# Kernel optimization log

Hardware: AMD Instinct MI355X
Metric: run time of the kernel (lower is better)

The kernel has to match this reference:

```python
import jax, jax.numpy as jnp
import numpy as np

DIM = 1024
NUM_HEADS = 16
WINDOW_SIZE = 512
HEAD_DIM = DIM // NUM_HEADS
SCALE = HEAD_DIM ** (-0.5)


def setup_inputs() -> dict:
    key = jax.random.key(0)
    kq, kk, kv = jax.random.split(key, 3)
    shape = (2, NUM_HEADS, 2048, HEAD_DIM)
    q = jax.random.normal(kq, shape, dtype=jnp.float32)
    k = jax.random.normal(kk, shape, dtype=jnp.float32)
    v = jax.random.normal(kv, shape, dtype=jnp.float32)
    return {"q": q, "k": k, "v": v}


def reference(q, k, v):
    B, H, N, D = q.shape
    pos = jnp.arange(N)
    # causal + sliding window: col <= row and col >= row - w + 1
    window_mask = (pos[None, :] <= pos[:, None]) & (pos[None, :] >= pos[:, None] - WINDOW_SIZE + 1)  # (N, N)
    attn = jnp.einsum("bhnd,bhmd->bhnm", q, k) * SCALE  # (B, H, N, N)
    attn = jnp.where(window_mask[None, None], attn, -jnp.inf)
    attn = jax.nn.softmax(attn, axis=-1)
    attn = jnp.nan_to_num(attn, nan=0.0)
    return jnp.einsum("bhnm,bhmd->bhnd", attn, v)
```

## Files before the change

### kernel.cpp

```cpp
#include <hip/hip_runtime.h>
#include <math.h>


#define SEQ 2048
#define HD  64
#define LDR 72

typedef short short8 __attribute__((ext_vector_type(8)));
typedef float f32x4  __attribute__((ext_vector_type(4)));

static __device__ inline unsigned short f2bf(float f){
  union{float f; unsigned u;} un; un.f=f;
  return (unsigned short)((un.u + 0x7FFFu + ((un.u>>16)&1u))>>16);
}
static __device__ inline int swz(int row){ return (row&3)|(((row>>3)&1)<<2); }

static __device__ __forceinline__ void gll16(const unsigned short* g, unsigned short* l){
  __builtin_amdgcn_global_load_lds(
    (const __attribute__((address_space(1))) unsigned int*)(const void*)g,
    (__attribute__((address_space(3))) unsigned int*)(void*)l, 16, 0, 0);
}

__global__ __launch_bounds__(256) void swa_prep(
    const float* __restrict__ k, const float* __restrict__ v,
    unsigned short* __restrict__ Kb, unsigned short* __restrict__ Vtb)
{
  const int tid=threadIdx.x, bid=blockIdx.x;
  const float C=0.18033688011112042f;

  if(bid<1024){
    const long tbase=(long)bid*4096;
    #pragma unroll
    for(int i=0;i<2;++i){
      int id=i*256+tid, r=id>>3, lc=id&7;
      float4 f0=*(const float4*)(k+tbase+r*64+lc*8);
      float4 f1=*(const float4*)(k+tbase+r*64+lc*8+4);
      unsigned short hh[8];
      hh[0]=f2bf(f0.x*C); hh[1]=f2bf(f0.y*C); hh[2]=f2bf(f0.z*C); hh[3]=f2bf(f0.w*C);
      hh[4]=f2bf(f1.x*C); hh[5]=f2bf(f1.y*C); hh[6]=f2bf(f1.z*C); hh[7]=f2bf(f1.w*C);
      *(uint4*)(Kb+tbase+r*64+(long)((lc^swz(r))*8))=*(uint4*)hh;
    }
  } else {
    __shared__ unsigned short Vs[64*68];
    const long tbase=(long)(bid-1024)*4096;
    #pragma unroll
    for(int i=0;i<2;++i){
      int id=i*256+tid, r=id>>3, c=id&7;
      int phys=(c^(r>>3))&7;
      float4 f0=*(const float4*)(v+tbase+r*64+c*8);
      float4 f1=*(const float4*)(v+tbase+r*64+c*8+4);
      ushort4 a,b;
      a.x=f2bf(f0.x); a.y=f2bf(f0.y); a.z=f2bf(f0.z); a.w=f2bf(f0.w);
      b.x=f2bf(f1.x); b.y=f2bf(f1.y); b.z=f2bf(f1.z); b.w=f2bf(f1.w);
      *(ushort4*)&Vs[r*68+phys*8]  =a;
      *(ushort4*)&Vs[r*68+phys*8+4]=b;
    }
    __syncthreads();
    #pragma unroll
    for(int i=0;i<2;++i){
      int id=i*256+tid, d=id>>3, lc=id&7;
      unsigned short t8[8];
      #pragma unroll
      for(int e=0;e<8;++e){
        int key=lc*8+e;
        int phys=((d>>3)^lc)&7;
        t8[e]=Vs[key*68 + phys*8 + (d&7)];
      }
      *(uint4*)(Vtb+tbase+d*64+(long)((lc^swz(d))*8))=*(uint4*)t8;
    }
  }
}

__global__ __launch_bounds__(512) void swa_main(
    const float* __restrict__ q,
    const unsigned short* __restrict__ Kb,
    const unsigned short* __restrict__ Vtb,
    float* __restrict__ out)
{
  __shared__ unsigned short Ks[2][8192];
  __shared__ unsigned short Vsh[2][8192];

  const int tid=threadIdx.x, bid=blockIdx.x;
  const int mt=bid&15, bh=bid>>4, m0=mt*128;
  const long base=(long)bh*SEQ*HD;
  const int wv=tid>>6, lane=tid&63, quad=lane>>4, l16=lane&15;
  const int qrow=m0+wv*16+l16;
  const int h=wv>>2;

  short8 qa[2];
  {
    const float* qp=q+base+(long)qrow*HD+quad*8;
    #pragma unroll
    for(int kk=0;kk<2;++kk){
      float4 f0=*(const float4*)(qp+kk*32);
      float4 f1=*(const float4*)(qp+kk*32+4);
      short8 a;
      a[0]=(short)f2bf(f0.x); a[1]=(short)f2bf(f0.y);
      a[2]=(short)f2bf(f0.z); a[3]=(short)f2bf(f0.w);
      a[4]=(short)f2bf(f1.x); a[5]=(short)f2bf(f1.y);
      a[6]=(short)f2bf(f1.z); a[7]=(short)f2bf(f1.w);
      qa[kk]=a;
    }
  }

  const int rbase=8*(l16>>2)+(l16&3);
  const int swk=(l16&3)|(((l16>>2)&1)<<2);
  const int swv=(l16&3)|(((l16>>3)&1)<<2);
  int kaoff[2][4], vboff[2][4];
  #pragma unroll
  for(int kk=0;kk<2;++kk){
    #pragma unroll
    for(int nt=0;nt<4;++nt)
      kaoff[kk][nt]=(rbase+(nt&1)*4+(nt>>1)*32)*64+(((quad+4*kk)^swk)*8);
    #pragma unroll
    for(int dt=0;dt<4;++dt)
      vboff[kk][dt]=(dt*16+l16)*64+(((quad+4*kk)^swv)*8);
  }

  const unsigned short* Kt=Kb +(long)bh*32*4096;
  const unsigned short* Vt=Vtb+(long)bh*32*4096;
  const int seg=tid*8;

  f32x4 oacc[4];
  #pragma unroll
  for(int dt=0;dt<4;++dt) oacc[dt]=(f32x4){0.f,0.f,0.f,0.f};
  float lrun=0.f;

  const int Tb  =2*mt+1;
  const int Tlo =(2*mt>8)?(2*mt-8):0;
  const int npairs=(Tb-Tlo+1)>>1;
  const int myTb=2*mt+h;
  const int myTlo=(myTb>=8)?(myTb-8):0;
  const bool clip=(myTb>=8);

  {
    const long o=(long)Tlo*4096;
    gll16(Kt+o+seg,      &Ks[0][seg]);
    gll16(Kt+o+4096+seg, &Ks[0][4096+seg]);
    gll16(Vt+o+seg,      &Vsh[0][seg]);
    gll16(Vt+o+4096+seg, &Vsh[0][4096+seg]);
  }
  __syncthreads();

  for(int p=0;p<npairs;++p){
    const int buf=p&1;
    if(p+1<npairs){
      const long o=(long)(Tlo+2*(p+1))*4096;
      gll16(Kt+o+seg,      &Ks[buf^1][seg]);
      gll16(Kt+o+4096+seg, &Ks[buf^1][4096+seg]);
      gll16(Vt+o+seg,      &Vsh[buf^1][seg]);
      gll16(Vt+o+4096+seg, &Vsh[buf^1][4096+seg]);
    }
    #pragma unroll
    for(int sub=0;sub<2;++sub){
      const int t=Tlo+2*p+sub;
      if(t>=myTlo && t<=myTb){
        const int tb_off=sub*4096;
        f32x4 sacc[4];
        #pragma unroll
        for(int nt=0;nt<4;++nt) sacc[nt]=(f32x4){0.f,0.f,0.f,0.f};
        #pragma unroll
        for(int kk=0;kk<2;++kk){
          #pragma unroll
          for(int nt=0;nt<4;++nt){
            short8 ka=*(const short8*)&Ks[buf][tb_off+kaoff[kk][nt]];
            sacc[nt]=__builtin_amdgcn_mfma_f32_16x16x32_bf16(ka,qa[kk],sacc[nt],0,0,0);
          }
        }
        short8 vb[4][2];
        #pragma unroll
        for(int dt=0;dt<4;++dt)
          #pragma unroll
          for(int kk=0;kk<2;++kk)
            vb[dt][kk]=*(const short8*)&Vsh[buf][tb_off+vboff[kk][dt]];

        unsigned short pb[16];
        const bool msk=(t==myTb)||(clip&&t==myTlo);
        if(msk){
          #pragma unroll
          for(int nt=0;nt<4;++nt){
            #pragma unroll
            for(int r=0;r<4;++r){
              float e=__builtin_amdgcn_exp2f(sacc[nt][r]);
              int key=t*64+8*quad+r+(nt&1)*4+(nt>>1)*32;
              bool valid=(key<=qrow)&&(key+511>=qrow);
              e=valid?e:0.f;
              lrun+=e;
              pb[nt*4+r]=f2bf(e);
            }
          }
        } else {
          #pragma unroll
          for(int nt=0;nt<4;++nt){
            #pragma unroll
            for(int r=0;r<4;++r){
              float e=__builtin_amdgcn_exp2f(sacc[nt][r]);
              lrun+=e;
              pb[nt*4+r]=f2bf(e);
            }
          }
        }
        short8 pa0,pa1;
        #pragma unroll
        for(int j=0;j<8;++j){ pa0[j]=(short)pb[j]; pa1[j]=(short)pb[8+j]; }
        #pragma unroll
        for(int dt=0;dt<4;++dt){
          oacc[dt]=__builtin_amdgcn_mfma_f32_16x16x32_bf16(pa0,vb[dt][0],oacc[dt],0,0,0);
          oacc[dt]=__builtin_amdgcn_mfma_f32_16x16x32_bf16(pa1,vb[dt][1],oacc[dt],0,0,0);
        }
      }
    }
    __syncthreads();
  }

  lrun+=__shfl_xor(lrun,16);
  lrun+=__shfl_xor(lrun,32);
  float linv=1.0f/lrun;
  #pragma unroll
  for(int r=0;r<4;++r){
    float lr=__shfl(linv,quad*4+r);
    const int orow=m0+wv*16+quad*4+r;
    #pragma unroll
    for(int dt=0;dt<4;++dt)
      out[base+(long)orow*HD+dt*16+l16]=oacc[dt][r]*lr;
  }
}

__global__ __launch_bounds__(256) void swa_fwd(
    const float* __restrict__ q, const float* __restrict__ k,
    const float* __restrict__ v, float* __restrict__ out)
{
  __shared__ short Qs[64*LDR];
  __shared__ short Ps[64*LDR];
  __shared__ short Ksh[2][64*LDR];
  __shared__ short Vtr[2][HD*LDR];

  const int tid=threadIdx.x, bid=blockIdx.x;
  const int mtile=bid&31, bh=bid>>5, m0=mtile*64;
  const long base=(long)bh*SEQ*HD;
  const int wv=tid>>6, lane=tid&63, quad=lane>>4, l16=lane&15;
  const int dcol=lane;

  {
    const float4* qg=(const float4*)(q+base+(long)m0*HD);
    #pragma unroll
    for(int i=0;i<4;++i){
      int idx=i*256+tid, r=idx>>4, c4=idx&15;
      float4 f=qg[idx];
      ushort4 hh; hh.x=f2bf(f.x); hh.y=f2bf(f.y); hh.z=f2bf(f.z); hh.w=f2bf(f.w);
      *(ushort4*)&Qs[r*LDR+c4*4]=hh;
    }
  }
  const int tb=mtile, tlo=(tb>8)?(tb-8):0;
  float4 kreg[4]; float vcol[4][4];
  {
    const float4* kg=(const float4*)(k+base+(long)(tlo*64)*HD);
    const float*  vg=v+base+(long)(tlo*64)*HD;
    #pragma unroll
    for(int i=0;i<4;++i) kreg[i]=kg[i*256+tid];
    #pragma unroll
    for(int g=0;g<4;++g){ int r0=wv*4+g*16;
      #pragma unroll
      for(int j=0;j<4;++j) vcol[g][j]=vg[(r0+j)*HD+dcol]; }
  }
  __syncthreads();
  short8 qa[2];
  #pragma unroll
  for(int kk=0;kk<2;++kk)
    qa[kk]=*(const short8*)&Qs[(wv*16+l16)*LDR+kk*32+quad*8];
  {
    #pragma unroll
    for(int i=0;i<4;++i){
      int idx=i*256+tid, r=idx>>4, c4=idx&15;
      float4 fk=kreg[i];
      ushort4 hk; hk.x=f2bf(fk.x); hk.y=f2bf(fk.y); hk.z=f2bf(fk.z); hk.w=f2bf(fk.w);
      *(ushort4*)&Ksh[0][r*LDR+c4*4]=hk;
    }
    #pragma unroll
    for(int g=0;g<4;++g){ int r0=wv*4+g*16;
      ushort4 hv; hv.x=f2bf(vcol[g][0]); hv.y=f2bf(vcol[g][1]);
                  hv.z=f2bf(vcol[g][2]); hv.w=f2bf(vcol[g][3]);
      *(ushort4*)&Vtr[0][dcol*LDR+r0]=hv; }
  }
  float lrun[4]={0.f,0.f,0.f,0.f};
  f32x4 oacc[4];
  #pragma unroll
  for(int dt=0;dt<4;++dt) oacc[dt]=(f32x4){0.f,0.f,0.f,0.f};
  __syncthreads();

  for(int t=tlo;t<=tb;++t){
    const int buf=(t-tlo)&1, j0=t*64;
    f32x4 sacc[4];
    #pragma unroll
    for(int nt=0;nt<4;++nt) sacc[nt]=(f32x4){0.f,0.f,0.f,0.f};
    #pragma unroll
    for(int kk=0;kk<2;++kk){
      #pragma unroll
      for(int nt=0;nt<4;++nt){
        short8 kb=*(const short8*)&Ksh[buf][(nt*16+l16)*LDR+kk*32+quad*8];
        sacc[nt]=__builtin_amdgcn_mfma_f32_16x16x32_bf16(qa[kk],kb,sacc[nt],0,0,0);
      }
    }
    if(t<tb){
      const float4* kg=(const float4*)(k+base+(long)((t+1)*64)*HD);
      const float*  vg=v+base+(long)((t+1)*64)*HD;
      #pragma unroll
      for(int i=0;i<4;++i) kreg[i]=kg[i*256+tid];
      #pragma unroll
      for(int g=0;g<4;++g){ int r0=wv*4+g*16;
        #pragma unroll
        for(int j=0;j<4;++j) vcol[g][j]=vg[(r0+j)*HD+dcol]; }
    }
    #pragma unroll
    for(int r=0;r<4;++r){
      const int grr=m0+wv*16+quad*4+r;
      #pragma unroll
      for(int nt=0;nt<4;++nt){
        const int gc=j0+nt*16+l16;
        float e=exp2f(sacc[nt][r]*0.18033688011112042f);
        float p=((gc<=grr)&&(gc>=grr-511))?e:0.f;
        lrun[r]+=p;
        Ps[(wv*16+quad*4+r)*LDR+nt*16+l16]=(short)f2bf(p);
      }
    }
    __syncthreads();
    #pragma unroll
    for(int kk=0;kk<2;++kk){
      short8 pa=*(const short8*)&Ps[(wv*16+l16)*LDR+kk*32+quad*8];
      #pragma unroll
      for(int dt=0;dt<4;++dt){
        short8 vb=*(const short8*)&Vtr[buf][(dt*16+l16)*LDR+kk*32+quad*8];
        oacc[dt]=__builtin_amdgcn_mfma_f32_16x16x32_bf16(pa,vb,oacc[dt],0,0,0);
      }
    }
    if(t<tb){
      #pragma unroll
      for(int i=0;i<4;++i){
        int idx=i*256+tid, r=idx>>4, c4=idx&15;
        float4 fk=kreg[i];
        ushort4 hk; hk.x=f2bf(fk.x); hk.y=f2bf(fk.y); hk.z=f2bf(fk.z); hk.w=f2bf(fk.w);
        *(ushort4*)&Ksh[buf^1][r*LDR+c4*4]=hk;
      }
      #pragma unroll
      for(int g=0;g<4;++g){ int r0=wv*4+g*16;
        ushort4 hv; hv.x=f2bf(vcol[g][0]); hv.y=f2bf(vcol[g][1]);
                    hv.z=f2bf(vcol[g][2]); hv.w=f2bf(vcol[g][3]);
        *(ushort4*)&Vtr[buf^1][dcol*LDR+r0]=hv; }
    }
    __syncthreads();
  }
  #pragma unroll
  for(int r=0;r<4;++r){
    float s=lrun[r];
    s+=__shfl_xor(s,1); s+=__shfl_xor(s,2); s+=__shfl_xor(s,4); s+=__shfl_xor(s,8);
    lrun[r]=(s>0.f)?(1.f/s):0.f;
  }
  #pragma unroll
  for(int r=0;r<4;++r){
    const int row=m0+wv*16+quad*4+r;
    #pragma unroll
    for(int dt=0;dt<4;++dt)
      out[base+(long)row*HD+dt*16+l16]=oacc[dt][r]*lrun[r];
  }
}

extern "C" void kernel_launch(void* const* d_in, const int* in_sizes, int n_in,
                              void* d_out, int out_size, void* d_ws, size_t ws_size,
                              hipStream_t stream) {
  (void)in_sizes; (void)n_in; (void)out_size;
  const float* q=(const float*)d_in[0];
  const float* k=(const float*)d_in[1];
  const float* v=(const float*)d_in[2];
  float* o=(float*)d_out;
  const size_t NEED = 2ull*32*2048*64*2;
  if (ws_size>=NEED){
    unsigned short* Kb =(unsigned short*)d_ws;
    unsigned short* Vtb=Kb+32ull*2048*64;
    hipLaunchKernelGGL(swa_prep, dim3(2048), dim3(256), 0, stream, k, v, Kb, Vtb);
    hipLaunchKernelGGL(swa_main, dim3(512),  dim3(512), 0, stream, q, Kb, Vtb, o);
  } else {
    hipLaunchKernelGGL(swa_fwd, dim3(1024), dim3(256), 0, stream, q, k, v, o);
  }
}
```

Measured before the change: 112.0 us.

## Give each wave two 16-row query sub-tiles to reuse K/V fragments

Each block now covers 256 query rows instead of 128, and each wave handles two 16-row sub-tiles. The K and V fragments are loaded from LDS once and reused for both sub-tiles. The float-to-bf16 conversion of P now truncates by packing the high halves instead of rounding. This halves LDS fragment loads per query row and K/V global traffic per block, but it also halves the grid to 256 blocks, which lowers parallelism on a 256-CU part, and it raises register pressure.

```diff
diff --git a/kernel.cpp b/kernel.cpp
--- a/kernel.cpp
+++ b/kernel.cpp
@@ -8,6 +8,7 @@
 
 typedef short short8 __attribute__((ext_vector_type(8)));
 typedef float f32x4  __attribute__((ext_vector_type(4)));
+typedef int   i32x4  __attribute__((ext_vector_type(4)));
 
 static __device__ inline unsigned short f2bf(float f){
   union{float f; unsigned u;} un; un.f=f;
@@ -81,15 +82,15 @@
   __shared__ unsigned short Vsh[2][8192];
 
   const int tid=threadIdx.x, bid=blockIdx.x;
-  const int mt=bid&15, bh=bid>>4, m0=mt*128;
+  const int mt=bid&7, bh=bid>>3, m0=mt*256;
   const long base=(long)bh*SEQ*HD;
   const int wv=tid>>6, lane=tid&63, quad=lane>>4, l16=lane&15;
-  const int qrow=m0+wv*16+l16;
-  const int h=wv>>2;
-
-  short8 qa[2];
-  {
-    const float* qp=q+base+(long)qrow*HD+quad*8;
+  const int qr0=m0+wv*32+l16;
+
+  short8 qa[2][2];
+  #pragma unroll
+  for(int s=0;s<2;++s){
+    const float* qp=q+base+(long)(qr0+s*16)*HD+quad*8;
     #pragma unroll
     for(int kk=0;kk<2;++kk){
       float4 f0=*(const float4*)(qp+kk*32);
@@ -99,7 +100,7 @@
       a[2]=(short)f2bf(f0.z); a[3]=(short)f2bf(f0.w);
       a[4]=(short)f2bf(f1.x); a[5]=(short)f2bf(f1.y);
       a[6]=(short)f2bf(f1.z); a[7]=(short)f2bf(f1.w);
-      qa[kk]=a;
+      qa[s][kk]=a;
     }
   }
 
@@ -121,17 +122,19 @@
   const unsigned short* Vt=Vtb+(long)bh*32*4096;
   const int seg=tid*8;
 
-  f32x4 oacc[4];
-  #pragma unroll
-  for(int dt=0;dt<4;++dt) oacc[dt]=(f32x4){0.f,0.f,0.f,0.f};
-  float lrun=0.f;
-
-  const int Tb  =2*mt+1;
-  const int Tlo =(2*mt>8)?(2*mt-8):0;
+  f32x4 oacc[2][4];
+  #pragma unroll
+  for(int s=0;s<2;++s)
+    #pragma unroll
+    for(int dt=0;dt<4;++dt) oacc[s][dt]=(f32x4){0.f,0.f,0.f,0.f};
+  float lrun[2]={0.f,0.f};
+
+  const int Tb =4*mt+3;
+  const int Tlo=(4*mt>8)?(4*mt-8):0;
   const int npairs=(Tb-Tlo+1)>>1;
-  const int myTb=2*mt+h;
-  const int myTlo=(myTb>=8)?(myTb-8):0;
+  const int myTb =4*mt+(wv>>1);
   const bool clip=(myTb>=8);
+  const int myTlo=clip?(myTb-8):0;
 
   {
     const long o=(long)Tlo*4096;
@@ -156,73 +159,84 @@
       const int t=Tlo+2*p+sub;
       if(t>=myTlo && t<=myTb){
         const int tb_off=sub*4096;
-        f32x4 sacc[4];
+        short8 ka[2][4], vb[4][2];
         #pragma unroll
-        for(int nt=0;nt<4;++nt) sacc[nt]=(f32x4){0.f,0.f,0.f,0.f};
+        for(int kk=0;kk<2;++kk)
+          #pragma unroll
+          for(int nt=0;nt<4;++nt)
+            ka[kk][nt]=*(const short8*)&Ks[buf][tb_off+kaoff[kk][nt]];
         #pragma unroll
-        for(int kk=0;kk<2;++kk){
+        for(int dt=0;dt<4;++dt)
+          #pragma unroll
+          for(int kk=0;kk<2;++kk)
+            vb[dt][kk]=*(const short8*)&Vsh[buf][tb_off+vboff[kk][dt]];
+
+        const bool msk=(t==myTb)||(clip&&t==myTlo);
+        #pragma unroll
+        for(int s=0;s<2;++s){
+          const int qrow=qr0+s*16;
+          f32x4 sacc[4];
+          #pragma unroll
+          for(int nt=0;nt<4;++nt) sacc[nt]=(f32x4){0.f,0.f,0.f,0.f};
+          #pragma unroll
+          for(int kk=0;kk<2;++kk)
+            #pragma unroll
+            for(int nt=0;nt<4;++nt)
+              sacc[nt]=__builtin_amdgcn_mfma_f32_16x16x32_bf16(ka[kk][nt],qa[s][kk],sacc[nt],0,0,0);
+
+          unsigned pp[8];
+          float ls=0.f;
           #pragma unroll
           for(int nt=0;nt<4;++nt){
-            short8 ka=*(const short8*)&Ks[buf][tb_off+kaoff[kk][nt]];
-            sacc[nt]=__builtin_amdgcn_mfma_f32_16x16x32_bf16(ka,qa[kk],sacc[nt],0,0,0);
+            float e0,e1,e2,e3;
+            e0=__builtin_amdgcn_exp2f(sacc[nt][0]);
+            e1=__builtin_amdgcn_exp2f(sacc[nt][1]);
+            e2=__builtin_amdgcn_exp2f(sacc[nt][2]);
+            e3=__builtin_amdgcn_exp2f(sacc[nt][3]);
+            if(msk){
+              const int kb0=t*64+8*quad+(nt&1)*4+(nt>>1)*32;
+              #pragma unroll
+              for(int r=0;r<4;++r){
+                const int key=kb0+r;
+                const bool valid=(key<=qrow)&&(key+511>=qrow);
+                float* ep=(r==0)?&e0:(r==1)?&e1:(r==2)?&e2:&e3;
+                *ep = valid ? *ep : 0.f;
+              }
+            }
+            ls+=e0+e1+e2+e3;
+            pp[nt*2+0]=(__float_as_uint(e1)&0xFFFF0000u)|(__float_as_uint(e0)>>16);
+            pp[nt*2+1]=(__float_as_uint(e3)&0xFFFF0000u)|(__float_as_uint(e2)>>16);
+          }
+          lrun[s]+=ls;
+          i32x4 i0={(int)pp[0],(int)pp[1],(int)pp[2],(int)pp[3]};
+          i32x4 i1={(int)pp[4],(int)pp[5],(int)pp[6],(int)pp[7]};
+          short8 pa0=*(short8*)&i0;
+          short8 pa1=*(short8*)&i1;
+          #pragma unroll
+          for(int dt=0;dt<4;++dt){
+            oacc[s][dt]=__builtin_amdgcn_mfma_f32_16x16x32_bf16(pa0,vb[dt][0],oacc[s][dt],0,0,0);
+            oacc[s][dt]=__builtin_amdgcn_mfma_f32_16x16x32_bf16(pa1,vb[dt][1],oacc[s][dt],0,0,0);
           }
         }
-        short8 vb[4][2];
-        #pragma unroll
-        for(int dt=0;dt<4;++dt)
-          #pragma unroll
-          for(int kk=0;kk<2;++kk)
-            vb[dt][kk]=*(const short8*)&Vsh[buf][tb_off+vboff[kk][dt]];
-
-        unsigned short pb[16];
-        const bool msk=(t==myTb)||(clip&&t==myTlo);
-        if(msk){
-          #pragma unroll
-          for(int nt=0;nt<4;++nt){
-            #pragma unroll
-            for(int r=0;r<4;++r){
-              float e=__builtin_amdgcn_exp2f(sacc[nt][r]);
-              int key=t*64+8*quad+r+(nt&1)*4+(nt>>1)*32;
-              bool valid=(key<=qrow)&&(key+511>=qrow);
-              e=valid?e:0.f;
-              lrun+=e;
-              pb[nt*4+r]=f2bf(e);
-            }
-          }
-        } else {
-          #pragma unroll
-          for(int nt=0;nt<4;++nt){
-            #pragma unroll
-            for(int r=0;r<4;++r){
-              float e=__builtin_amdgcn_exp2f(sacc[nt][r]);
-              lrun+=e;
-              pb[nt*4+r]=f2bf(e);
-            }
-          }
-        }
-        short8 pa0,pa1;
-        #pragma unroll
-        for(int j=0;j<8;++j){ pa0[j]=(short)pb[j]; pa1[j]=(short)pb[8+j]; }
-        #pragma unroll
-        for(int dt=0;dt<4;++dt){
-          oacc[dt]=__builtin_amdgcn_mfma_f32_16x16x32_bf16(pa0,vb[dt][0],oacc[dt],0,0,0);
-          oacc[dt]=__builtin_amdgcn_mfma_f32_16x16x32_bf16(pa1,vb[dt][1],oacc[dt],0,0,0);
-        }
       }
     }
     __syncthreads();
   }
 
-  lrun+=__shfl_xor(lrun,16);
-  lrun+=__shfl_xor(lrun,32);
-  float linv=1.0f/lrun;
-  #pragma unroll
-  for(int r=0;r<4;++r){
-    float lr=__shfl(linv,quad*4+r);
-    const int orow=m0+wv*16+quad*4+r;
-    #pragma unroll
-    for(int dt=0;dt<4;++dt)
-      out[base+(long)orow*HD+dt*16+l16]=oacc[dt][r]*lr;
+  #pragma unroll
+  for(int s=0;s<2;++s){
+    float l=lrun[s];
+    l+=__shfl_xor(l,16);
+    l+=__shfl_xor(l,32);
+    float linv=1.0f/l;
+    #pragma unroll
+    for(int r=0;r<4;++r){
+      float lr=__shfl(linv,quad*4+r);
+      const int orow=m0+wv*32+s*16+quad*4+r;
+      #pragma unroll
+      for(int dt=0;dt<4;++dt)
+        out[base+(long)orow*HD+dt*16+l16]=oacc[s][dt][r]*lr;
+    }
   }
 }
 
@@ -377,7 +391,7 @@
     unsigned short* Kb =(unsigned short*)d_ws;
     unsigned short* Vtb=Kb+32ull*2048*64;
     hipLaunchKernelGGL(swa_prep, dim3(2048), dim3(256), 0, stream, k, v, Kb, Vtb);
-    hipLaunchKernelGGL(swa_main, dim3(512),  dim3(512), 0, stream, q, Kb, Vtb, o);
+    hipLaunchKernelGGL(swa_main, dim3(256),  dim3(512), 0, stream, q, Kb, Vtb, o);
   } else {
     hipLaunchKernelGGL(swa_fwd, dim3(1024), dim3(256), 0, stream, q, k, v, o);
   }
```

After: 114.3 us. 1.02x slower.
